# Optimization experiments

Hardware: AMD Instinct MI355X
Metric: run time of the kernel (lower is better)

Reference implementation:

```python
import jax, jax.numpy as jnp
import numpy as np
import math

M = 0.5
S = 64.0
TH = math.cos(math.pi - M)           # threshold cos(pi - m)
MM = math.sin(math.pi - M) * M       # sin(pi - m) * m
EPS = 1e-12

def _l2norm(x, axis=-1):
    return x / jnp.sqrt(jnp.sum(x * x, axis=axis, keepdims=True) + EPS)

def setup_inputs() -> dict:
    key = jax.random.key(0)
    k1, k2, k3 = jax.random.split(key, 3)
    B, D, C = 512, 512, 100000
    features = jax.random.normal(k1, (B, D), dtype=jnp.float32)
    weight = jax.random.normal(k2, (C, D), dtype=jnp.float32)
    labels = jax.random.randint(k3, (B,), 0, C, dtype=jnp.int32)
    return {"features": features, "labels": labels, "weight": weight}

def reference(features, labels, weight):
    # cos_theta: [B, C] = normalized features @ normalized weight^T
    cos_theta = jnp.einsum('bd,cd->bc', _l2norm(features), _l2norm(weight))
    cos_theta = jnp.clip(cos_theta, -1.0, 1.0)
    B = features.shape[0]
    rows = jnp.arange(B)
    # margin correction only affects the target column per row; gather it
    tgt_cos = cos_theta[rows, labels]                      # [B]
    theta_m = jnp.arccos(tgt_cos) + M
    cos_theta_m = jnp.cos(theta_m)
    tgt_adj = jnp.where(tgt_cos > TH, cos_theta_m, tgt_cos - MM)
    output = cos_theta.at[rows, labels].set(tgt_adj)
    return S * output
```

## Files before the change

### kernel.cpp

```cpp
#include <hip/hip_runtime.h>
#include <hip/hip_bf16.h>


typedef __attribute__((ext_vector_type(8))) short short8;
typedef __attribute__((ext_vector_type(8))) unsigned short u16x8;
typedef __attribute__((ext_vector_type(4))) float f32x4;

#define TH_CONST  (-0.8775825618903728f)
#define MM_CONST  (0.23971276930210156f)
#define M_MARGIN  0.5f
#define S_SCALE   64.0f

#define BM 128
#define BN 128
#define BK 32
#define KD 512

__device__ __forceinline__ unsigned short f2bf(float x) {
    unsigned int u = __float_as_uint(x);
    u += 0x7fffu + ((u >> 16) & 1u);
    return (unsigned short)(u >> 16);
}

__global__ __launch_bounds__(256, 2)
void arcface_kernel(const float* __restrict__ F,
                    const int*   __restrict__ labels,
                    const float* __restrict__ W,
                    float*       __restrict__ Out,
                    const int C)
{
    __shared__ unsigned short As[BM][BK];
    __shared__ unsigned short Bs[BN][BK];
    __shared__ float normF[BM];
    __shared__ float normW[BN];
    __shared__ int   Ls[BM];

    const int t = threadIdx.x;
    const int m_base = blockIdx.x * BM;
    const int n_base = blockIdx.y * BN;

    if (t < BM) Ls[t] = labels[m_base + t];

    const int r = t >> 1;
    const int h = t & 1;

    const int lane = t & 63;
    const int wave = t >> 6;
    const int wm = (wave >> 1) * 64;
    const int wn = (wave & 1) * 64;
    const int quad = lane >> 4;
    const int lcol = lane & 15;

    f32x4 acc[4][4];
    #pragma unroll
    for (int i = 0; i < 4; ++i)
        #pragma unroll
        for (int j = 0; j < 4; ++j)
            acc[i][j] = (f32x4){0.f, 0.f, 0.f, 0.f};

    const int cls = n_base + r;
    const bool cvalid = (cls < C);

    const float* Arow = F + (size_t)(m_base + r) * KD + h * 16;
    const float* Wrow = W + (size_t)(cvalid ? cls : 0) * KD + h * 16;

    float sF = 0.f, sW = 0.f;

    for (int kt = 0; kt < KD / BK; ++kt) {
        const float4* ap = (const float4*)(Arow + kt * BK);
        const float4* wp = (const float4*)(Wrow + kt * BK);
        float4 a0 = ap[0], a1 = ap[1], a2 = ap[2], a3 = ap[3];
        float4 w0, w1, w2, w3;
        if (cvalid) { w0 = wp[0]; w1 = wp[1]; w2 = wp[2]; w3 = wp[3]; }
        else {
            w0 = make_float4(0.f,0.f,0.f,0.f); w1 = w0; w2 = w0; w3 = w0;
        }

        sF += a0.x*a0.x + a0.y*a0.y + a0.z*a0.z + a0.w*a0.w
            + a1.x*a1.x + a1.y*a1.y + a1.z*a1.z + a1.w*a1.w
            + a2.x*a2.x + a2.y*a2.y + a2.z*a2.z + a2.w*a2.w
            + a3.x*a3.x + a3.y*a3.y + a3.z*a3.z + a3.w*a3.w;
        sW += w0.x*w0.x + w0.y*w0.y + w0.z*w0.z + w0.w*w0.w
            + w1.x*w1.x + w1.y*w1.y + w1.z*w1.z + w1.w*w1.w
            + w2.x*w2.x + w2.y*w2.y + w2.z*w2.z + w2.w*w2.w
            + w3.x*w3.x + w3.y*w3.y + w3.z*w3.z + w3.w*w3.w;

        u16x8 pa0, pa1, pb0, pb1;
        pa0[0]=f2bf(a0.x); pa0[1]=f2bf(a0.y); pa0[2]=f2bf(a0.z); pa0[3]=f2bf(a0.w);
        pa0[4]=f2bf(a1.x); pa0[5]=f2bf(a1.y); pa0[6]=f2bf(a1.z); pa0[7]=f2bf(a1.w);
        pa1[0]=f2bf(a2.x); pa1[1]=f2bf(a2.y); pa1[2]=f2bf(a2.z); pa1[3]=f2bf(a2.w);
        pa1[4]=f2bf(a3.x); pa1[5]=f2bf(a3.y); pa1[6]=f2bf(a3.z); pa1[7]=f2bf(a3.w);
        pb0[0]=f2bf(w0.x); pb0[1]=f2bf(w0.y); pb0[2]=f2bf(w0.z); pb0[3]=f2bf(w0.w);
        pb0[4]=f2bf(w1.x); pb0[5]=f2bf(w1.y); pb0[6]=f2bf(w1.z); pb0[7]=f2bf(w1.w);
        pb1[0]=f2bf(w2.x); pb1[1]=f2bf(w2.y); pb1[2]=f2bf(w2.z); pb1[3]=f2bf(w2.w);
        pb1[4]=f2bf(w3.x); pb1[5]=f2bf(w3.y); pb1[6]=f2bf(w3.z); pb1[7]=f2bf(w3.w);

        __syncthreads();
        *((u16x8*)&As[r][h*16])     = pa0;
        *((u16x8*)&As[r][h*16 + 8]) = pa1;
        *((u16x8*)&Bs[r][h*16])     = pb0;
        *((u16x8*)&Bs[r][h*16 + 8]) = pb1;
        __syncthreads();

        short8 af[4], bfr[4];
        #pragma unroll
        for (int i = 0; i < 4; ++i) {
            af[i]  = *(const short8*)&As[wm + i*16 + lcol][quad*8];
            bfr[i] = *(const short8*)&Bs[wn + i*16 + lcol][quad*8];
        }
        #pragma unroll
        for (int i = 0; i < 4; ++i)
            #pragma unroll
            for (int j = 0; j < 4; ++j)
                acc[i][j] = __builtin_amdgcn_mfma_f32_16x16x32_bf16(
                                af[i], bfr[j], acc[i][j], 0, 0, 0);
    }

    sF += __shfl_xor(sF, 1);
    sW += __shfl_xor(sW, 1);
    if (h == 0) {
        normF[r] = 1.0f / sqrtf(sF + 1e-12f);
        normW[r] = 1.0f / sqrtf(sW + 1e-12f);
    }
    __syncthreads();

    #pragma unroll
    for (int mi = 0; mi < 4; ++mi) {
        const int rl_base = wm + mi*16 + quad*4;
        #pragma unroll
        for (int rg = 0; rg < 4; ++rg) {
            const int rl = rl_base + rg;
            const float invf = normF[rl];
            const int lbl = Ls[rl];
            float* orow = Out + (size_t)(m_base + rl) * C;
            #pragma unroll
            for (int ni = 0; ni < 4; ++ni) {
                const int cl = wn + ni*16 + lcol;
                const int gcol = n_base + cl;
                if (gcol < C) {
                    float v = acc[mi][ni][rg] * invf * normW[cl];
                    v = fminf(1.0f, fmaxf(-1.0f, v));
                    if (gcol == lbl) {
                        v = (v > TH_CONST) ? cosf(acosf(v) + M_MARGIN)
                                           : (v - MM_CONST);
                    }
                    orow[gcol] = S_SCALE * v;
                }
            }
        }
    }
}

extern "C" void kernel_launch(void* const* d_in, const int* in_sizes, int n_in,
                              void* d_out, int out_size, void* d_ws, size_t ws_size,
                              hipStream_t stream) {
    const float* F      = (const float*)d_in[0];
    const int*   labels = (const int*)d_in[1];
    const float* W      = (const float*)d_in[2];
    float*       Out    = (float*)d_out;

    const int B = in_sizes[1];
    const int C = in_sizes[2] / KD;

    dim3 grid(B / BM, (C + BN - 1) / BN);
    arcface_kernel<<<grid, dim3(256), 0, stream>>>(F, labels, W, Out, C);
}
```

Baseline: 445.5 us.

## Prefetch next K tile, use fp16 packed conversion, pad LDS, swizzle block order

```diff
diff --git a/kernel.cpp b/kernel.cpp
--- a/kernel.cpp
+++ b/kernel.cpp
@@ -2,8 +2,8 @@
 #include <hip/hip_bf16.h>
 
 
-typedef __attribute__((ext_vector_type(8))) short short8;
-typedef __attribute__((ext_vector_type(8))) unsigned short u16x8;
+typedef __attribute__((ext_vector_type(8))) __fp16 half8;
+typedef __attribute__((ext_vector_type(2))) __fp16 half2v;
 typedef __attribute__((ext_vector_type(4))) float f32x4;
 
 #define TH_CONST  (-0.8775825618903728f)
@@ -15,11 +15,29 @@
 #define BN 128
 #define BK 32
 #define KD 512
+#define LDK 40
 
-__device__ __forceinline__ unsigned short f2bf(float x) {
-    unsigned int u = __float_as_uint(x);
-    u += 0x7fffu + ((u >> 16) & 1u);
-    return (unsigned short)(u >> 16);
+union H8 { half2v h2[4]; half8 h8; };
+
+__device__ __forceinline__ void cvt16(H8& lo, H8& hi,
+                                      const float4& x0, const float4& x1,
+                                      const float4& x2, const float4& x3) {
+    lo.h2[0] = __builtin_amdgcn_cvt_pkrtz(x0.x, x0.y);
+    lo.h2[1] = __builtin_amdgcn_cvt_pkrtz(x0.z, x0.w);
+    lo.h2[2] = __builtin_amdgcn_cvt_pkrtz(x1.x, x1.y);
+    lo.h2[3] = __builtin_amdgcn_cvt_pkrtz(x1.z, x1.w);
+    hi.h2[0] = __builtin_amdgcn_cvt_pkrtz(x2.x, x2.y);
+    hi.h2[1] = __builtin_amdgcn_cvt_pkrtz(x2.z, x2.w);
+    hi.h2[2] = __builtin_amdgcn_cvt_pkrtz(x3.x, x3.y);
+    hi.h2[3] = __builtin_amdgcn_cvt_pkrtz(x3.z, x3.w);
+}
+
+__device__ __forceinline__ float sq16(const float4& x0, const float4& x1,
+                                      const float4& x2, const float4& x3) {
+    return x0.x*x0.x + x0.y*x0.y + x0.z*x0.z + x0.w*x0.w
+         + x1.x*x1.x + x1.y*x1.y + x1.z*x1.z + x1.w*x1.w
+         + x2.x*x2.x + x2.y*x2.y + x2.z*x2.z + x2.w*x2.w
+         + x3.x*x3.x + x3.y*x3.y + x3.z*x3.z + x3.w*x3.w;
 }
 
 __global__ __launch_bounds__(256, 2)
@@ -27,18 +45,32 @@
                     const int*   __restrict__ labels,
                     const float* __restrict__ W,
                     float*       __restrict__ Out,
-                    const int C)
+                    const int C, const int MB, const int NB)
 {
-    __shared__ unsigned short As[BM][BK];
-    __shared__ unsigned short Bs[BN][BK];
+    __shared__ __fp16 As[BM][LDK];
+    __shared__ __fp16 Bs[BN][LDK];
     __shared__ float normF[BM];
     __shared__ float normW[BN];
     __shared__ int   Ls[BM];
 
+    const int id = blockIdx.x;
+    const int group = 8 * MB;
+    const int full  = (NB / 8) * group;
+    int m_idx, n_idx;
+    if (id < full) {
+        const int chunk = id / group, pos = id % group;
+        n_idx = chunk * 8 + (pos & 7);
+        m_idx = pos >> 3;
+    } else {
+        const int tail = NB - (NB / 8) * 8;
+        const int r2 = id - full;
+        n_idx = (NB / 8) * 8 + (r2 % tail);
+        m_idx = r2 / tail;
+    }
+    const int m_base = m_idx * BM;
+    const int n_base = n_idx * BN;
+
     const int t = threadIdx.x;
-    const int m_base = blockIdx.x * BM;
-    const int n_base = blockIdx.y * BN;
-
     if (t < BM) Ls[t] = labels[m_base + t];
 
     const int r = t >> 1;
@@ -66,53 +98,47 @@
 
     float sF = 0.f, sW = 0.f;
 
+    float4 a0, a1, a2, a3, w0, w1, w2, w3;
+    {
+        const float4* ap = (const float4*)(Arow);
+        const float4* wp = (const float4*)(Wrow);
+        a0 = ap[0]; a1 = ap[1]; a2 = ap[2]; a3 = ap[3];
+        if (cvalid) { w0 = wp[0]; w1 = wp[1]; w2 = wp[2]; w3 = wp[3]; }
+        else { w0 = make_float4(0.f,0.f,0.f,0.f); w1 = w0; w2 = w0; w3 = w0; }
+    }
+
     for (int kt = 0; kt < KD / BK; ++kt) {
-        const float4* ap = (const float4*)(Arow + kt * BK);
-        const float4* wp = (const float4*)(Wrow + kt * BK);
-        float4 a0 = ap[0], a1 = ap[1], a2 = ap[2], a3 = ap[3];
-        float4 w0, w1, w2, w3;
-        if (cvalid) { w0 = wp[0]; w1 = wp[1]; w2 = wp[2]; w3 = wp[3]; }
-        else {
-            w0 = make_float4(0.f,0.f,0.f,0.f); w1 = w0; w2 = w0; w3 = w0;
+        sF += sq16(a0, a1, a2, a3);
+        sW += sq16(w0, w1, w2, w3);
+        H8 ua0, ua1, ub0, ub1;
+        cvt16(ua0, ua1, a0, a1, a2, a3);
+        cvt16(ub0, ub1, w0, w1, w2, w3);
+
+        __syncthreads();
+        *(half8*)&As[r][h*16]     = ua0.h8;
+        *(half8*)&As[r][h*16 + 8] = ua1.h8;
+        *(half8*)&Bs[r][h*16]     = ub0.h8;
+        *(half8*)&Bs[r][h*16 + 8] = ub1.h8;
+        __syncthreads();
+
+        if (kt + 1 < KD / BK) {
+            const float4* ap = (const float4*)(Arow + (kt + 1) * BK);
+            const float4* wp = (const float4*)(Wrow + (kt + 1) * BK);
+            a0 = ap[0]; a1 = ap[1]; a2 = ap[2]; a3 = ap[3];
+            if (cvalid) { w0 = wp[0]; w1 = wp[1]; w2 = wp[2]; w3 = wp[3]; }
         }
 
-        sF += a0.x*a0.x + a0.y*a0.y + a0.z*a0.z + a0.w*a0.w
-            + a1.x*a1.x + a1.y*a1.y + a1.z*a1.z + a1.w*a1.w
-            + a2.x*a2.x + a2.y*a2.y + a2.z*a2.z + a2.w*a2.w
-            + a3.x*a3.x + a3.y*a3.y + a3.z*a3.z + a3.w*a3.w;
-        sW += w0.x*w0.x + w0.y*w0.y + w0.z*w0.z + w0.w*w0.w
-            + w1.x*w1.x + w1.y*w1.y + w1.z*w1.z + w1.w*w1.w
-            + w2.x*w2.x + w2.y*w2.y + w2.z*w2.z + w2.w*w2.w
-            + w3.x*w3.x + w3.y*w3.y + w3.z*w3.z + w3.w*w3.w;
-
-        u16x8 pa0, pa1, pb0, pb1;
-        pa0[0]=f2bf(a0.x); pa0[1]=f2bf(a0.y); pa0[2]=f2bf(a0.z); pa0[3]=f2bf(a0.w);
-        pa0[4]=f2bf(a1.x); pa0[5]=f2bf(a1.y); pa0[6]=f2bf(a1.z); pa0[7]=f2bf(a1.w);
-        pa1[0]=f2bf(a2.x); pa1[1]=f2bf(a2.y); pa1[2]=f2bf(a2.z); pa1[3]=f2bf(a2.w);
-        pa1[4]=f2bf(a3.x); pa1[5]=f2bf(a3.y); pa1[6]=f2bf(a3.z); pa1[7]=f2bf(a3.w);
-        pb0[0]=f2bf(w0.x); pb0[1]=f2bf(w0.y); pb0[2]=f2bf(w0.z); pb0[3]=f2bf(w0.w);
-        pb0[4]=f2bf(w1.x); pb0[5]=f2bf(w1.y); pb0[6]=f2bf(w1.z); pb0[7]=f2bf(w1.w);
-        pb1[0]=f2bf(w2.x); pb1[1]=f2bf(w2.y); pb1[2]=f2bf(w2.z); pb1[3]=f2bf(w2.w);
-        pb1[4]=f2bf(w3.x); pb1[5]=f2bf(w3.y); pb1[6]=f2bf(w3.z); pb1[7]=f2bf(w3.w);
-
-        __syncthreads();
-        *((u16x8*)&As[r][h*16])     = pa0;
-        *((u16x8*)&As[r][h*16 + 8]) = pa1;
-        *((u16x8*)&Bs[r][h*16])     = pb0;
-        *((u16x8*)&Bs[r][h*16 + 8]) = pb1;
-        __syncthreads();
-
-        short8 af[4], bfr[4];
+        half8 af[4], bfr[4];
         #pragma unroll
         for (int i = 0; i < 4; ++i) {
-            af[i]  = *(const short8*)&As[wm + i*16 + lcol][quad*8];
-            bfr[i] = *(const short8*)&Bs[wn + i*16 + lcol][quad*8];
+            af[i]  = *(const half8*)&As[wm + i*16 + lcol][quad*8];
+            bfr[i] = *(const half8*)&Bs[wn + i*16 + lcol][quad*8];
         }
         #pragma unroll
         for (int i = 0; i < 4; ++i)
             #pragma unroll
             for (int j = 0; j < 4; ++j)
-                acc[i][j] = __builtin_amdgcn_mfma_f32_16x16x32_bf16(
+                acc[i][j] = __builtin_amdgcn_mfma_f32_16x16x32_f16(
                                 af[i], bfr[j], acc[i][j], 0, 0, 0);
     }
 
@@ -161,7 +187,8 @@
 
     const int B = in_sizes[1];
     const int C = in_sizes[2] / KD;
+    const int MB = B / BM;
+    const int NB = (C + BN - 1) / BN;
 
-    dim3 grid(B / BM, (C + BN - 1) / BN);
-    arcface_kernel<<<grid, dim3(256), 0, stream>>>(F, labels, W, Out, C);
+    arcface_kernel<<<dim3(MB * NB), dim3(256), 0, stream>>>(F, labels, W, Out, C, MB, NB);
 }
```

After: 454.0 us. Within noise of the previous version (+1.9%).
